# Kernel tuning notes

Measured on AMD Instinct MI355X. Metric: run time of the kernel, lower is better.

Reference implementation:

```python
import jax, jax.numpy as jnp
import numpy as np

DIM = 1024
HEADS = 16
HEAD_DIM = DIM // HEADS
SCALE = DIM ** -0.5  # note: original uses full dim, not head_dim


def setup_inputs() -> dict:
    key = jax.random.key(0)
    k1, k2, k3, k4 = jax.random.split(key, 4)
    x = jax.random.normal(k1, (4, 2048, DIM), dtype=jnp.float32)
    # nn.Linear(dim, 3*dim, bias=False): weight [3*dim, dim]; y = x @ W.T
    w_qkv = jax.random.normal(k2, (3 * DIM, DIM), dtype=jnp.float32) * (DIM ** -0.5)
    w_out = jax.random.normal(k3, (DIM, DIM), dtype=jnp.float32) * (DIM ** -0.5)
    b_out = jax.random.normal(k4, (DIM,), dtype=jnp.float32) * 0.01
    return {"x": x, "w_qkv": w_qkv, "w_out": w_out, "b_out": b_out}


def reference(x, w_qkv, w_out, b_out):
    b, n, d = x.shape
    qkv = jnp.einsum('bnd,ed->bne', x, w_qkv)  # [b, n, 3*dim]
    # rearrange 'b n (qkv h d) -> qkv b h n d'
    qkv = qkv.reshape(b, n, 3, HEADS, HEAD_DIM).transpose(2, 0, 3, 1, 4)
    q, k, v = qkv[0], qkv[1], qkv[2]
    dots = jnp.einsum('bhid,bhjd->bhij', q, k) * SCALE
    attn = jax.nn.softmax(dots, axis=-1)
    out = jnp.einsum('bhij,bhjd->bhid', attn, v)
    out = out.transpose(0, 2, 1, 3).reshape(b, n, d)  # b h n d -> b n (h d)
    return jnp.einsum('bnd,ed->bne', out, w_out) + b_out
```

## Files before the change

kernel.cpp:

```cpp
#include <hip/hip_runtime.h>
#include <stdint.h>
#include <stddef.h>

typedef _Float16 f16;
typedef __attribute__((ext_vector_type(8))) _Float16 f16x8;
typedef __attribute__((ext_vector_type(4))) _Float16 f16x4;
typedef __attribute__((ext_vector_type(4))) float f32x4;

#define DINL __device__ __forceinline__

DINL void async_cp16(void* lds, const void* gmem) {
    __builtin_amdgcn_global_load_lds(
        (const __attribute__((address_space(1))) void*)(uintptr_t)gmem,
        (__attribute__((address_space(3))) void*)(uint32_t)(uintptr_t)lds,
        16, 0, 0);
}

__global__ void cast_fused(const float* __restrict__ x, f16* __restrict__ xh,
                           const float* __restrict__ wq, f16* __restrict__ wqh,
                           const float* __restrict__ wo, f16* __restrict__ woh,
                           float qs) {
    int stride = gridDim.x * blockDim.x;
    for (int i = blockIdx.x * blockDim.x + threadIdx.x; i < 3145728; i += stride) {
        const float4* src; f16x4* dst; float s = 1.f;
        if (i < 2097152)      { src = (const float4*)x  + i;            dst = (f16x4*)xh  + i; }
        else if (i < 2883584) { int j = i - 2097152; src = (const float4*)wq + j; dst = (f16x4*)wqh + j;
                                if (j < 262144) s = qs; }
        else                  { int j = i - 2883584; src = (const float4*)wo + j; dst = (f16x4*)woh + j; }
        float4 v = *src;
        f16x4 h = { (f16)(v.x * s), (f16)(v.y * s), (f16)(v.z * s), (f16)(v.w * s) };
        *dst = h;
    }
}

template <typename TC, bool HAS_BIAS>
__global__ __launch_bounds__(256) void gemm_bt(
    const f16* __restrict__ A, const f16* __restrict__ B,
    TC* __restrict__ C, const float* __restrict__ bias,
    int M, int N, int K)
{
    constexpr int BK = 64;
    __shared__ __align__(16) f16 As[128 * BK];
    __shared__ __align__(16) f16 Bs[128 * BK];

    const int tid  = threadIdx.x;
    const int lane = tid & 63;
    const int wave = tid >> 6;
    const int bm = blockIdx.y * 128;
    const int bn = blockIdx.x * 128;
    const int wr = (wave >> 1) * 64;
    const int wc = (wave & 1) * 64;

    f32x4 acc[4][4] = {};

    for (int k0 = 0; k0 < K; k0 += BK) {
#pragma unroll
        for (int it = 0; it < 4; ++it) {
            int s = tid + it * 256, row = s >> 3, cc = (s & 7) ^ (row & 7);
            async_cp16(&As[(size_t)s * 8], &A[(size_t)(bm + row) * K + k0 + cc * 8]);
        }
#pragma unroll
        for (int it = 0; it < 4; ++it) {
            int s = tid + it * 256, row = s >> 3, cc = (s & 7) ^ (row & 7);
            async_cp16(&Bs[(size_t)s * 8], &B[(size_t)(bn + row) * K + k0 + cc * 8]);
        }
        __syncthreads();

#pragma unroll
        for (int ks = 0; ks < BK; ks += 32) {
            const int rlo = lane & 15;
            const int c = (ks >> 3) + (lane >> 4);
            f16x8 af[4], bf[4];
#pragma unroll
            for (int m = 0; m < 4; ++m) {
                int r = wr + m * 16 + rlo;
                af[m] = *(const f16x8*)&As[(r * 8 + (c ^ (r & 7))) * 8];
            }
#pragma unroll
            for (int n = 0; n < 4; ++n) {
                int r = wc + n * 16 + rlo;
                bf[n] = *(const f16x8*)&Bs[(r * 8 + (c ^ (r & 7))) * 8];
            }
#pragma unroll
            for (int m = 0; m < 4; ++m)
#pragma unroll
                for (int n = 0; n < 4; ++n)
                    acc[m][n] = __builtin_amdgcn_mfma_f32_16x16x32_f16(af[m], bf[n], acc[m][n], 0, 0, 0);
        }
        __syncthreads();
    }

#pragma unroll
    for (int n = 0; n < 4; ++n) {
        const int gc = bn + wc + n * 16 + (lane & 15);
        float bv = 0.f;
        if constexpr (HAS_BIAS) bv = bias[gc];
#pragma unroll
        for (int m = 0; m < 4; ++m) {
            const int gr0 = bm + wr + m * 16 + ((lane >> 4) << 2);
#pragma unroll
            for (int r = 0; r < 4; ++r) {
                float v = acc[m][n][r] + bv;
                if constexpr (sizeof(TC) == 4) C[(size_t)(gr0 + r) * N + gc] = v;
                else                           C[(size_t)(gr0 + r) * N + gc] = (f16)v;
            }
        }
    }
}

__global__ __launch_bounds__(256) void transpose_v(const f16* __restrict__ qkv, f16* __restrict__ vt) {
    __shared__ float T[64][65];
    const int bid = blockIdx.x, bh = bid >> 5, st = bid & 31;
    const int b = bh >> 4, h = bh & 15, s0 = st * 64;
    const int tid = threadIdx.x;
    const int rs = tid >> 2, c0 = (tid & 3) * 16;
    const f16* src = &qkv[(size_t)(b * 2048 + s0 + rs) * 3072 + 2048 + h * 64 + c0];
    f16x8 v0 = ((const f16x8*)src)[0], v1 = ((const f16x8*)src)[1];
#pragma unroll
    for (int e = 0; e < 8; ++e) { T[rs][c0 + e] = (float)v0[e]; T[rs][c0 + 8 + e] = (float)v1[e]; }
    __syncthreads();
    const int rd = tid >> 2, k0 = (tid & 3) * 16;
    f16x8 w0, w1;
#pragma unroll
    for (int e = 0; e < 8; ++e) { w0[e] = (f16)T[k0 + e][rd]; w1[e] = (f16)T[k0 + 8 + e][rd]; }
    f16* dst = &vt[(size_t)(bh * 64 + rd) * 2048 + s0 + k0];
    ((f16x8*)dst)[0] = w0; ((f16x8*)dst)[1] = w1;
}

DINL int phi_row(int r) {
    return (r & 32) | ((r & 12) << 1) | ((r & 16) >> 2) | (r & 3);
}

__global__ __launch_bounds__(256, 4) void attn_mfma(
    const f16* __restrict__ qkv, const f16* __restrict__ vt, f16* __restrict__ out)
{
    constexpr int TD = 3072;
    constexpr int KSTR = 64 * TD;
    __shared__ __align__(16) f16 Ks[2][64 * 64];
    __shared__ __align__(16) f16 Vs[2][64 * 64];

    const int tid = threadIdx.x, lane = tid & 63, wave = tid >> 6;
    const int bh = blockIdx.x, b = bh >> 4, h = bh & 15;
    const int q0 = blockIdx.y * 128;
    const size_t base = (size_t)b * 2048 * TD + h * 64;
    const int lo = lane & 15, hi = lane >> 4;

    f16x8 qf[2][2];
#pragma unroll
    for (int g = 0; g < 2; ++g) {
        const f16* qp = &qkv[base + (size_t)(q0 + wave * 32 + g * 16 + lo) * TD + hi * 8];
        qf[g][0] = *(const f16x8*)qp;
        qf[g][1] = *(const f16x8*)(qp + 32);
    }

    const int s1 = tid,        r1 = s1 >> 3, c1 = (s1 & 7) ^ (r1 & 7);
    const int s2 = tid + 256,  r2 = s2 >> 3, c2 = (s2 & 7) ^ (r2 & 7);
    const f16* kg1 = &qkv[base + 1024 + (size_t)phi_row(r1) * TD + c1 * 8];
    const f16* kg2 = &qkv[base + 1024 + (size_t)phi_row(r2) * TD + c2 * 8];
    const f16* vg1 = &vt[(size_t)(bh * 64 + r1) * 2048 + c1 * 8];
    const f16* vg2 = &vt[(size_t)(bh * 64 + r2) * 2048 + c2 * 8];
    f16* kd1 = &Ks[0][s1 * 8]; f16* kd2 = &Ks[0][s2 * 8];
    f16* vd1 = &Vs[0][s1 * 8]; f16* vd2 = &Vs[0][s2 * 8];

    async_cp16(kd1, kg1); async_cp16(kd2, kg2);
    async_cp16(vd1, vg1); async_cp16(vd2, vg2);
    kg1 += KSTR; kg2 += KSTR; vg1 += 64; vg2 += 64;

    float lsum[2] = {};
    f32x4 o_[2][4] = {};

    for (int jt = 0; jt < 32; ++jt) {
        const int cur = jt & 1;
        __syncthreads();
        if (jt + 1 < 32) {
            const int nb = (cur ^ 1) * 4096;
            async_cp16(kd1 + nb, kg1); async_cp16(kd2 + nb, kg2);
            async_cp16(vd1 + nb, vg1); async_cp16(vd2 + nb, vg2);
            kg1 += KSTR; kg2 += KSTR; vg1 += 64; vg2 += 64;
        }

        f32x4 sc[2][4] = {{}, {}};
#pragma unroll
        for (int ks = 0; ks < 2; ++ks) {
            const int c = ks * 4 + hi;
#pragma unroll
            for (int n = 0; n < 4; ++n) {
                int kr = n * 16 + lo;
                f16x8 kf = *(const f16x8*)&Ks[cur][(kr * 8 + (c ^ (kr & 7))) * 8];
                sc[0][n] = __builtin_amdgcn_mfma_f32_16x16x32_f16(kf, qf[0][ks], sc[0][n], 0, 0, 0);
                sc[1][n] = __builtin_amdgcn_mfma_f32_16x16x32_f16(kf, qf[1][ks], sc[1][n], 0, 0, 0);
            }
        }

        f16x8 pa[2][2];
#pragma unroll
        for (int g = 0; g < 2; ++g)
#pragma unroll
        for (int n = 0; n < 4; ++n) {
            float p0 = exp2f(sc[g][n][0]), p1 = exp2f(sc[g][n][1]);
            float p2 = exp2f(sc[g][n][2]), p3 = exp2f(sc[g][n][3]);
            lsum[g] += (p0 + p1) + (p2 + p3);
            const int off = (n & 1) * 4;
            const int w = n >> 1;
            pa[g][w][off]   = (f16)p0; pa[g][w][off+1] = (f16)p1;
            pa[g][w][off+2] = (f16)p2; pa[g][w][off+3] = (f16)p3;
        }

#pragma unroll
        for (int ks = 0; ks < 2; ++ks) {
            const int c = ks * 4 + hi;
#pragma unroll
            for (int n = 0; n < 4; ++n) {
                int dd = n * 16 + lo;
                f16x8 vb = *(const f16x8*)&Vs[cur][(dd * 8 + (c ^ (dd & 7))) * 8];
                o_[0][n] = __builtin_amdgcn_mfma_f32_16x16x32_f16(pa[0][ks], vb, o_[0][n], 0, 0, 0);
                o_[1][n] = __builtin_amdgcn_mfma_f32_16x16x32_f16(pa[1][ks], vb, o_[1][n], 0, 0, 0);
            }
        }
    }

#pragma unroll
    for (int g = 0; g < 2; ++g) {
        float ls = lsum[g];
        ls += __shfl_xor(ls, 16);
        ls += __shfl_xor(ls, 32);
#pragma unroll
        for (int r = 0; r < 4; ++r) {
            float inv = 1.f / __shfl(ls, hi * 4 + r);
            int row = q0 + wave * 32 + g * 16 + hi * 4 + r;
#pragma unroll
            for (int n = 0; n < 4; ++n) {
                int dim = h * 64 + n * 16 + lo;
                out[(size_t)(b * 2048 + row) * 1024 + dim] = (f16)(o_[g][n][r] * inv);
            }
        }
    }
}

extern "C" void kernel_launch(void* const* d_in, const int* in_sizes, int n_in,
                              void* d_out, int out_size, void* d_ws, size_t ws_size,
                              hipStream_t stream)
{
    int ix = 0, iq = 1, iw = 2, ib = 3;
    for (int i = 0; i < n_in; ++i) {
        if      (in_sizes[i] == 8388608) ix = i;
        else if (in_sizes[i] == 3145728) iq = i;
        else if (in_sizes[i] == 1048576) iw = i;
        else if (in_sizes[i] == 1024)    ib = i;
    }
    const float* x     = (const float*)d_in[ix];
    const float* w_qkv = (const float*)d_in[iq];
    const float* w_out = (const float*)d_in[iw];
    const float* b_out = (const float*)d_in[ib];

    char* ws = (char*)d_ws;
    f16* Xh    = (f16*)(ws + 0);
    f16* AOh   = Xh;
    f16* Wqkvh = (f16*)(ws + 16777216);
    f16* QKVh  = (f16*)(ws + 23068672);
    f16* Vth   = (f16*)(ws + 73400320);
    f16* Wouth = (f16*)(ws + 90177536);

    const float QSCALE = 0.03125f * 1.4426950408889634f;

    cast_fused<<<3072, 256, 0, stream>>>(x, Xh, w_qkv, Wqkvh, w_out, Wouth, QSCALE);

    gemm_bt<f16, false><<<dim3(24, 64), 256, 0, stream>>>(
        Xh, Wqkvh, QKVh, nullptr, 8192, 3072, 1024);

    transpose_v<<<2048, 256, 0, stream>>>(QKVh, Vth);

    attn_mfma<<<dim3(64, 16), 256, 0, stream>>>(QKVh, Vth, AOh);

    gemm_bt<float, true><<<dim3(8, 64), 256, 0, stream>>>(
        AOh, Wouth, (float*)d_out, b_out, 8192, 1024, 1024);
}
```

Baseline: 297.2 us.

## Rewrite GEMM as 8-wave 256x128 tile with 4-stage async LDS pipeline

The GEMM kernel becomes 512 threads computing 256x128 tiles with BK=32. A 4-stage ring of asynchronous global-to-LDS copies is controlled by explicit vmcnt waits and a single barrier per step, replacing the load-sync-compute-sync loop. This is meant to hide global memory latency and cut barrier overhead. s_setprio is also placed around the MFMA blocks in both the GEMM and attention kernels to favour matrix issue. The cost is 96KB of LDS per block, which limits occupancy, plus fragile hand-tuned wait counts.

```diff
diff --git a/kernel.cpp b/kernel.cpp
--- a/kernel.cpp
+++ b/kernel.cpp
@@ -34,70 +34,93 @@
 }
 
 template <typename TC, bool HAS_BIAS>
-__global__ __launch_bounds__(256) void gemm_bt(
+__global__ __launch_bounds__(512, 2) void gemm8p(
     const f16* __restrict__ A, const f16* __restrict__ B,
     TC* __restrict__ C, const float* __restrict__ bias,
     int M, int N, int K)
 {
-    constexpr int BK = 64;
-    __shared__ __align__(16) f16 As[128 * BK];
-    __shared__ __align__(16) f16 Bs[128 * BK];
+    __shared__ __align__(16) char lds[98304];
 
     const int tid  = threadIdx.x;
     const int lane = tid & 63;
     const int wave = tid >> 6;
-    const int bm = blockIdx.y * 128;
-    const int bn = blockIdx.x * 128;
-    const int wr = (wave >> 1) * 64;
-    const int wc = (wave & 1) * 64;
+    const int rlo  = lane & 15;
+    const int hi   = lane >> 4;
+    const int wm   = wave & 3;
+    const int wn   = wave >> 2;
+    const int bm   = blockIdx.y * 256;
+    const int bn   = blockIdx.x * 128;
+
+    const int rA = tid >> 2;
+    const int lc = (tid & 3) ^ ((tid >> 3) & 3);
+    const f16* pA0 = A + (size_t)(bm + rA) * K + lc * 8;
+    const f16* pA1 = A + (size_t)(bm + 128 + rA) * K + lc * 8;
+    const f16* pB  = B + (size_t)(bn + rA) * K + lc * 8;
+    const uint32_t dst0 = (uint32_t)tid * 16;
+    const uint32_t dst1 = 8192u + (uint32_t)tid * 16;
+    const uint32_t dstB = (uint32_t)tid * 16;
+
+    const int fsw = (rlo >> 1) & 3;
+    uint32_t afb[4], bfb[4];
+#pragma unroll
+    for (int m = 0; m < 4; ++m)
+        afb[m] = (uint32_t)(wm * 64 + m * 16 + rlo) * 64 + (uint32_t)((hi ^ fsw) << 4);
+#pragma unroll
+    for (int n = 0; n < 4; ++n)
+        bfb[n] = (uint32_t)(wn * 64 + n * 16 + rlo) * 64 + (uint32_t)((hi ^ fsw) << 4);
 
     f32x4 acc[4][4] = {};
-
-    for (int k0 = 0; k0 < K; k0 += BK) {
-#pragma unroll
-        for (int it = 0; it < 4; ++it) {
-            int s = tid + it * 256, row = s >> 3, cc = (s & 7) ^ (row & 7);
-            async_cp16(&As[(size_t)s * 8], &A[(size_t)(bm + row) * K + k0 + cc * 8]);
-        }
-#pragma unroll
-        for (int it = 0; it < 4; ++it) {
-            int s = tid + it * 256, row = s >> 3, cc = (s & 7) ^ (row & 7);
-            async_cp16(&Bs[(size_t)s * 8], &B[(size_t)(bn + row) * K + k0 + cc * 8]);
-        }
-        __syncthreads();
-
-#pragma unroll
-        for (int ks = 0; ks < BK; ks += 32) {
-            const int rlo = lane & 15;
-            const int c = (ks >> 3) + (lane >> 4);
-            f16x8 af[4], bf[4];
-#pragma unroll
-            for (int m = 0; m < 4; ++m) {
-                int r = wr + m * 16 + rlo;
-                af[m] = *(const f16x8*)&As[(r * 8 + (c ^ (r & 7))) * 8];
-            }
-#pragma unroll
-            for (int n = 0; n < 4; ++n) {
-                int r = wc + n * 16 + rlo;
-                bf[n] = *(const f16x8*)&Bs[(r * 8 + (c ^ (r & 7))) * 8];
-            }
-#pragma unroll
-            for (int m = 0; m < 4; ++m)
-#pragma unroll
-                for (int n = 0; n < 4; ++n)
-                    acc[m][n] = __builtin_amdgcn_mfma_f32_16x16x32_f16(af[m], bf[n], acc[m][n], 0, 0, 0);
-        }
-        __syncthreads();
+    const int NP = K >> 5;
+
+    auto stage = [&](int sg) {
+        const uint32_t sa = (uint32_t)(sg & 3) << 14;
+        const uint32_t sb = 65536u + ((uint32_t)(sg & 3) << 13);
+        async_cp16(lds + sa + dst0, pA0);
+        async_cp16(lds + sa + dst1, pA1);
+        async_cp16(lds + sb + dstB, pB);
+        pA0 += 32; pA1 += 32; pB += 32;
+    };
+
+    stage(0); stage(1); stage(2);
+
+    for (int g = 0; g < NP; ++g) {
+        if (g + 2 < NP)      asm volatile("s_waitcnt vmcnt(6)" ::: "memory");
+        else if (g + 1 < NP) asm volatile("s_waitcnt vmcnt(3)" ::: "memory");
+        else                 asm volatile("s_waitcnt vmcnt(0)" ::: "memory");
+        __builtin_amdgcn_s_barrier();
+        asm volatile("" ::: "memory");
+        __builtin_amdgcn_sched_barrier(0);
+
+        if (g + 3 < NP) stage(g + 3);
+
+        const uint32_t sa = (uint32_t)(g & 3) << 14;
+        const uint32_t sb = 65536u + ((uint32_t)(g & 3) << 13);
+
+        f16x8 af[4], bf[4];
+#pragma unroll
+        for (int m = 0; m < 4; ++m)
+            af[m] = *(const f16x8*)(lds + sa + afb[m]);
+#pragma unroll
+        for (int n = 0; n < 4; ++n)
+            bf[n] = *(const f16x8*)(lds + sb + bfb[n]);
+
+        __builtin_amdgcn_s_setprio(1);
+#pragma unroll
+        for (int m = 0; m < 4; ++m)
+#pragma unroll
+            for (int n = 0; n < 4; ++n)
+                acc[m][n] = __builtin_amdgcn_mfma_f32_16x16x32_f16(af[m], bf[n], acc[m][n], 0, 0, 0);
+        __builtin_amdgcn_s_setprio(0);
     }
 
 #pragma unroll
     for (int n = 0; n < 4; ++n) {
-        const int gc = bn + wc + n * 16 + (lane & 15);
+        const int gc = bn + wn * 64 + n * 16 + rlo;
         float bv = 0.f;
         if constexpr (HAS_BIAS) bv = bias[gc];
 #pragma unroll
         for (int m = 0; m < 4; ++m) {
-            const int gr0 = bm + wr + m * 16 + ((lane >> 4) << 2);
+            const int gr0 = bm + wm * 64 + m * 16 + (hi << 2);
 #pragma unroll
             for (int r = 0; r < 4; ++r) {
                 float v = acc[m][n][r] + bv;
@@ -180,6 +203,7 @@
         }
 
         f32x4 sc[2][4] = {{}, {}};
+        __builtin_amdgcn_s_setprio(1);
 #pragma unroll
         for (int ks = 0; ks < 2; ++ks) {
             const int c = ks * 4 + hi;
@@ -191,6 +215,7 @@
                 sc[1][n] = __builtin_amdgcn_mfma_f32_16x16x32_f16(kf, qf[1][ks], sc[1][n], 0, 0, 0);
             }
         }
+        __builtin_amdgcn_s_setprio(0);
 
         f16x8 pa[2][2];
 #pragma unroll
@@ -206,6 +231,7 @@
             pa[g][w][off+2] = (f16)p2; pa[g][w][off+3] = (f16)p3;
         }
 
+        __builtin_amdgcn_s_setprio(1);
 #pragma unroll
         for (int ks = 0; ks < 2; ++ks) {
             const int c = ks * 4 + hi;
@@ -217,6 +243,7 @@
                 o_[1][n] = __builtin_amdgcn_mfma_f32_16x16x32_f16(pa[1][ks], vb, o_[1][n], 0, 0, 0);
             }
         }
+        __builtin_amdgcn_s_setprio(0);
     }
 
 #pragma unroll
@@ -265,13 +292,13 @@
 
     cast_fused<<<3072, 256, 0, stream>>>(x, Xh, w_qkv, Wqkvh, w_out, Wouth, QSCALE);
 
-    gemm_bt<f16, false><<<dim3(24, 64), 256, 0, stream>>>(
+    gemm8p<f16, false><<<dim3(24, 32), 512, 0, stream>>>(
         Xh, Wqkvh, QKVh, nullptr, 8192, 3072, 1024);
 
     transpose_v<<<2048, 256, 0, stream>>>(QKVh, Vth);
 
     attn_mfma<<<dim3(64, 16), 256, 0, stream>>>(QKVh, Vth, AOh);
 
-    gemm_bt<float, true><<<dim3(8, 64), 256, 0, stream>>>(
+    gemm8p<float, true><<<dim3(8, 32), 512, 0, stream>>>(
         AOh, Wouth, (float*)d_out, b_out, 8192, 1024, 1024);
 }
```

After: 290.1 us. -2.4%, faster.
